# Optimization experiments

Measured on AMD Instinct MI355X. Metric: run time of the kernel, lower is better.

The kernel has to match this reference:

```python
import jax, jax.numpy as jnp
import numpy as np

B, T_ENC, T_DEC = 32, 256, 256
ENC, HID, ATT, CCH, K = 512, 1024, 128, 32, 31
OUT, PRE = 80, 256
ZONEOUT = 0.1
P_DROP = 0.5
PAD = (K - 1) // 2


def setup_inputs() -> dict:
    key = jax.random.key(0)
    ks = jax.random.split(key, 20)
    def n(k, shape, s=0.02):
        return jax.random.normal(k, shape, dtype=jnp.float32) * s
    inp = {}
    inp["encoder_outs"] = jax.random.normal(ks[0], (B, T_ENC, ENC), dtype=jnp.float32)
    inp["decoder_targets"] = jax.random.normal(ks[1], (B, T_DEC, OUT), dtype=jnp.float32)
    keep = 1.0 - P_DROP
    # pre-sampled inverted-dropout masks for the 2 prenet layers at every step
    inp["prenet_masks"] = jax.random.bernoulli(ks[2], keep, (T_DEC, 2, B, PRE)).astype(jnp.float32) / keep
    inp["in_lens"] = jax.random.randint(ks[3], (B,), T_ENC // 2, T_ENC + 1, dtype=jnp.int32)
    # location-sensitive attention params
    inp["V_w"] = n(ks[4], (ATT, ENC)); inp["V_b"] = jnp.zeros((ATT,), jnp.float32)
    inp["W_w"] = n(ks[5], (ATT, HID))
    inp["U_w"] = n(ks[6], (ATT, CCH))
    inp["F_w"] = n(ks[7], (CCH, 1, K))
    inp["w_w"] = n(ks[8], (1, ATT)); inp["w_b"] = jnp.zeros((1,), jnp.float32)
    # prenet
    inp["pre_w0"] = n(ks[9], (PRE, OUT)); inp["pre_b0"] = jnp.zeros((PRE,), jnp.float32)
    inp["pre_w1"] = n(ks[10], (PRE, PRE)); inp["pre_b1"] = jnp.zeros((PRE,), jnp.float32)
    # stacked LSTM cells (zoneout wrappers)
    inp["l0_wih"] = n(ks[11], (4 * HID, ENC + PRE)); inp["l0_whh"] = n(ks[12], (4 * HID, HID))
    inp["l0_bih"] = jnp.zeros((4 * HID,), jnp.float32); inp["l0_bhh"] = jnp.zeros((4 * HID,), jnp.float32)
    inp["l1_wih"] = n(ks[13], (4 * HID, HID)); inp["l1_whh"] = n(ks[14], (4 * HID, HID))
    inp["l1_bih"] = jnp.zeros((4 * HID,), jnp.float32); inp["l1_bhh"] = jnp.zeros((4 * HID,), jnp.float32)
    # output projections
    inp["feat_w"] = n(ks[15], (OUT, ENC + HID))
    inp["prob_w"] = n(ks[16], (1, ENC + HID)); inp["prob_b"] = jnp.zeros((1,), jnp.float32)
    return inp


def _lstm_cell(x, h, c, wih, whh, bih, bhh):
    g = x @ wih.T + bih + h @ whh.T + bhh
    i, f, gg, o = jnp.split(g, 4, axis=1)  # torch LSTMCell gate order
    c2 = jax.nn.sigmoid(f) * c + jax.nn.sigmoid(i) * jnp.tanh(gg)
    h2 = jax.nn.sigmoid(o) * jnp.tanh(c2)
    return h2, c2


def _decode(encoder_outs, decoder_targets, prenet_masks, in_lens,
            V_w, V_b, W_w, U_w, F_w, w_w, w_b,
            pre_w0, pre_b0, pre_w1, pre_b1,
            l0_wih, l0_whh, l0_bih, l0_bhh,
            l1_wih, l1_whh, l1_bih, l1_bhh,
            feat_w, prob_w, prob_b):
    b = encoder_outs.shape[0]
    pad_mask = jnp.arange(T_ENC)[None, :] >= in_lens[:, None]       # [B,T_enc] True = pad
    att_uniform = (~pad_mask).astype(jnp.float32) / in_lens[:, None].astype(jnp.float32)
    processed_memory = encoder_outs @ V_w.T + V_b                   # [B,T_enc,ATT]
    neg = jnp.float32(-1e9)

    # teacher forcing: prev_out at step 0 is the go-frame, then target[t-1]
    targets_prev = jnp.concatenate(
        [jnp.zeros((b, 1, OUT), jnp.float32), decoder_targets[:, :-1]], axis=1)
    xs = (jnp.swapaxes(targets_prev, 0, 1), prenet_masks[:, 0], prenet_masks[:, 1],
          jnp.arange(T_DEC))

    def step(carry, x):
        h0, c0, h1, c1, cum = carry
        prev_out, m0, m1, t = x
        # location-sensitive attention (prev_att_w = None at t=0 -> uniform over valid)
        att_prev = jnp.where(t == 0, att_uniform, cum)              # [B,T_enc]
        f = jax.lax.conv_general_dilated(
            att_prev[:, None, :], F_w, (1,), [(PAD, PAD)],
            dimension_numbers=("NCH", "OIH", "NCH"))                # [B,CCH,T_enc]
        f = jnp.swapaxes(f, 1, 2)                                   # [B,T_enc,CCH]
        erg = jnp.tanh(processed_memory + (h0 @ W_w.T)[:, None, :] + f @ U_w.T)
        erg = (erg @ w_w.T + w_b)[..., 0]                           # [B,T_enc]
        erg = jnp.where(pad_mask, neg, erg)
        aw = jax.nn.softmax(erg, axis=1)
        att_c = jnp.einsum("bt,bte->be", aw, encoder_outs)          # [B,ENC]
        # prenet (dropout always on, via pre-sampled masks)
        p = jax.nn.relu(prev_out @ pre_w0.T + pre_b0) * m0
        p = jax.nn.relu(p @ pre_w1.T + pre_b1) * m1
        xin = jnp.concatenate([att_c, p], axis=1)
        # zoneout LSTM stack (eval-mode zoneout: convex mix of prev/new states)
        h0n, c0n = _lstm_cell(xin, h0, c0, l0_wih, l0_whh, l0_bih, l0_bhh)
        h0 = ZONEOUT * h0 + (1.0 - ZONEOUT) * h0n
        c0 = ZONEOUT * c0 + (1.0 - ZONEOUT) * c0n
        h1n, c1n = _lstm_cell(h0, h1, c1, l1_wih, l1_whh, l1_bih, l1_bhh)
        h1 = ZONEOUT * h1 + (1.0 - ZONEOUT) * h1n
        c1 = ZONEOUT * c1 + (1.0 - ZONEOUT) * c1n
        hcs = jnp.concatenate([h1, att_c], axis=1)                  # [B,HID+ENC]
        out = hcs @ feat_w.T                                        # [B,OUT] (no bias)
        logit = hcs @ prob_w.T + prob_b                             # [B,1]
        return (h0, c0, h1, c1, cum + aw), (out, logit, aw)

    z = jnp.zeros((b, HID), jnp.float32)
    carry0 = (z, z, z, z, jnp.zeros((b, T_ENC), jnp.float32))
    _, (outs, logits, att_ws) = jax.lax.scan(step, carry0, xs)
    outs = jnp.transpose(outs, (1, 2, 0))      # [B,OUT,T_dec]
    logits = logits[..., 0].T                  # [B,T_dec]
    att_ws = jnp.swapaxes(att_ws, 0, 1)        # [B,T_dec,T_enc]
    return outs, logits, att_ws


def reference(encoder_outs, decoder_targets, prenet_masks, in_lens,
              V_w, V_b, W_w, U_w, F_w, w_w, w_b,
              pre_w0, pre_b0, pre_w1, pre_b1,
              l0_wih, l0_whh, l0_bih, l0_bhh,
              l1_wih, l1_whh, l1_bih, l1_bhh,
              feat_w, prob_w, prob_b):
    return _decode(encoder_outs, decoder_targets, prenet_masks, in_lens,
                   V_w, V_b, W_w, U_w, F_w, w_w, w_b,
                   pre_w0, pre_b0, pre_w1, pre_b1,
                   l0_wih, l0_whh, l0_bih, l0_bhh,
                   l1_wih, l1_whh, l1_bih, l1_bhh,
                   feat_w, prob_w, prob_b)
```

## Files before the change

### kernel.cpp

```cpp
#include <hip/hip_runtime.h>

typedef _Float16 half2_t __attribute__((ext_vector_type(2)));
typedef unsigned uint_t;

#define B_    32
#define TE_   256
#define TD_   256
#define ENC_  512
#define HID_  1024
#define ATT_  128
#define OUT_  80
#define PRE_  256

#define LOG_OFF  655360u
#define ATTW_OFF 663552u

#define OFF_PM    0u
#define OFF_P1H   1048576u
#define OFF_M     2097152u
#define OFF_WWH   2101248u
#define OFF_ENCH  2166784u
#define OFF_W0P   4263936u
#define OFF_W1P   7933952u
#define OFF_XC0   12128256u
#define OFF_XC1   12173312u
#define OFF_C0    12206080u
#define OFF_C1    12238848u
#define OFF_CUM   12271616u
#define OFF_ATTC  12279808u
#define OFF_END   12328960u

__device__ __forceinline__ float rcp_f(float x){ return __builtin_amdgcn_rcpf(x); }
__device__ __forceinline__ float sigm(float x){ return rcp_f(1.0f + __expf(-x)); }
__device__ __forceinline__ float tanh_f(float x){ float e = __expf(2.0f*x); return 1.0f - 2.0f*rcp_f(e+1.0f); }

__device__ __forceinline__ uint_t packh2(float a, float b){
  half2_t h; h[0] = (_Float16)a; h[1] = (_Float16)b;
  return __builtin_bit_cast(uint_t, h);
}
__device__ __forceinline__ float dot2f(uint_t w, uint_t x, float c){
#if __has_builtin(__builtin_amdgcn_fdot2)
  return __builtin_amdgcn_fdot2(__builtin_bit_cast(half2_t, w),
                                __builtin_bit_cast(half2_t, x), c, false);
#else
  half2_t a = __builtin_bit_cast(half2_t, w), b = __builtin_bit_cast(half2_t, x);
  return c + (float)a[0]*(float)b[0] + (float)a[1]*(float)b[1];
#endif
}


__global__ void k_init(float* __restrict__ ws){
  unsigned n = OFF_END - OFF_XC0;
  for (unsigned i = blockIdx.x*blockDim.x + threadIdx.x; i < n; i += gridDim.x*blockDim.x)
    ws[OFF_XC0 + i] = 0.f;
}

__global__ void k_precm(const float* __restrict__ Uw, const float* __restrict__ Fw,
                        float* __restrict__ ws){
  float* M = ws + OFF_M;
  for (int idx = threadIdx.x; idx < 128*31; idx += blockDim.x){
    int a = idx / 31, k = idx % 31;
    float s = 0.f;
    for (int c = 0; c < 32; c++) s += Uw[a*32+c]*Fw[c*31+k];
    M[idx] = s;
  }
}

__global__ void k_cvtww(const float* __restrict__ Ww, float* __restrict__ ws){
  uint_t* WWH = (uint_t*)(ws + OFF_WWH);
  int a = blockIdx.x;
  for (int p = threadIdx.x; p < 512; p += blockDim.x)
    WWH[a*512 + p] = packh2(Ww[a*1024 + 2*p], Ww[a*1024 + 2*p + 1]);
}

__global__ void k_packenc(const float* __restrict__ enc, float* __restrict__ ws){
  uint_t* ENCH = (uint_t*)(ws + OFF_ENCH);
  size_t row = blockIdx.x;
  for (int j = threadIdx.x; j < 256; j += blockDim.x)
    ENCH[row*256 + j] = packh2(enc[row*512 + 2*j], enc[row*512 + 2*j + 1]);
}

__global__ void k_packw0(const float* __restrict__ wih, const float* __restrict__ whh,
                         float* __restrict__ ws){
  uint_t* W = (uint_t*)(ws + OFF_W0P);
  size_t r = blockIdx.x;
  for (int p = threadIdx.x; p < 896; p += blockDim.x){
    int k = 2*p;
    const float* src = (k < 768) ? (wih + r*768 + k) : (whh + r*1024 + (k-768));
    W[r*896 + p] = packh2(src[0], src[1]);
  }
}

__global__ void k_packw1(const float* __restrict__ wih, const float* __restrict__ whh,
                         float* __restrict__ ws){
  uint_t* W = (uint_t*)(ws + OFF_W1P);
  size_t r = blockIdx.x;
  for (int p = threadIdx.x; p < 1024; p += blockDim.x){
    int k = 2*p;
    const float* src = (k < 1024) ? (wih + r*1024 + k) : (whh + r*1024 + (k-1024));
    W[r*1024 + p] = packh2(src[0], src[1]);
  }
}

__global__ __launch_bounds__(256) void k_pm(const float* __restrict__ enc,
    const float* __restrict__ Vw, const float* __restrict__ Vb, float* __restrict__ ws){
  float* pm = ws + OFF_PM;
  int b  = blockIdx.x >> 2;
  int s0 = (blockIdx.x & 3) << 6;
  int a  = threadIdx.x & 127;
  int sh = threadIdx.x >> 7;
  __shared__ float Vl[128*65];
  __shared__ float El[64*64];
  float acc[32];
  #pragma unroll
  for (int i=0;i<32;i++) acc[i]=0.f;
  for (int kc=0; kc<ENC_; kc+=64){
    for (int i=threadIdx.x; i<128*64; i+=256){
      int aa = i>>6, kk = i&63;
      Vl[aa*65+kk] = Vw[aa*ENC_ + kc + kk];
    }
    for (int i=threadIdx.x; i<64*64; i+=256){
      int ss = i>>6, kk = i&63;
      El[i] = enc[(size_t)(b*TE_ + s0 + ss)*ENC_ + kc + kk];
    }
    __syncthreads();
    for (int k=0;k<64;k++){
      float va = Vl[a*65+k];
      const float* er = &El[(sh*32)*64 + k];
      #pragma unroll
      for (int s=0;s<32;s++) acc[s] += va * er[s*64];
    }
    __syncthreads();
  }
  float bb = Vb[a];
  for (int s=0;s<32;s++)
    pm[((size_t)b*128 + a)*256 + (s0 + sh*32 + s)] = acc[s] + bb;
}

__global__ __launch_bounds__(256) void k_pre(const float* __restrict__ tgt,
    const float* __restrict__ w0, const float* __restrict__ b0,
    const float* __restrict__ w1, const float* __restrict__ b1,
    const float* __restrict__ masks, float* __restrict__ ws){
  uint_t* P1H = (uint_t*)(ws + OFF_P1H);
  int t = blockIdx.x, j = threadIdx.x;
  __shared__ float xl[32*80];
  __shared__ float p0l[32*256];
  __shared__ float p1s[256*32];
  for (int i=j; i<32*80; i+=256){
    int b = i/80, o = i%80;
    xl[i] = (t==0) ? 0.f : tgt[((size_t)b*TD_ + (t-1))*80 + o];
  }
  __syncthreads();
  {
    float bj = b0[j];
    float w[80];
    #pragma unroll
    for (int o=0;o<80;o++) w[o] = w0[j*80+o];
    for (int b=0;b<32;b++){
      float a0=0,a1=0,a2=0,a3=0;
      const float* x = &xl[b*80];
      #pragma unroll
      for (int o=0;o<80;o+=4){
        a0+=w[o]*x[o]; a1+=w[o+1]*x[o+1]; a2+=w[o+2]*x[o+2]; a3+=w[o+3]*x[o+3];
      }
      float m = masks[(((size_t)t*2+0)*32+b)*256 + j];
      p0l[b*256 + j] = fmaxf(bj+a0+a1+a2+a3, 0.f) * m;
    }
  }
  __syncthreads();
  {
    float bj = b1[j];
    const float4* wr = (const float4*)(w1 + j*256);
    float acc[32];
    #pragma unroll
    for (int i=0;i<32;i++) acc[i]=0.f;
    for (int o4=0;o4<64;o4++){
      float4 w = wr[o4];
      #pragma unroll
      for (int b=0;b<32;b++){
        const float4 xv = *(const float4*)&p0l[b*256 + o4*4];
        acc[b] += w.x*xv.x + w.y*xv.y + w.z*xv.z + w.w*xv.w;
      }
    }
    for (int b=0;b<32;b++){
      float m = masks[(((size_t)t*2+1)*32+b)*256 + j];
      p1s[j*32 + b] = fmaxf(bj+acc[b], 0.f) * m;
    }
  }
  __syncthreads();
  for (int i=j; i<32*128; i+=256){
    int b = i >> 7, jp = i & 127;
    P1H[((size_t)t*32 + b)*128 + jp] = packh2(p1s[(2*jp)*32 + b], p1s[(2*jp+1)*32 + b]);
  }
}


__global__ __launch_bounds__(512) void k_stepa(int t,
    const int* __restrict__ lens, const float* __restrict__ ww, const float* __restrict__ wb,
    const float* __restrict__ featw, const float* __restrict__ probw,
    const float* __restrict__ probb, float* __restrict__ ws, float* __restrict__ out){
  __shared__ __align__(16) uint_t h0l[512];
  __shared__ __align__(16) float Ml[128*32];
  __shared__ __align__(16) float apad[320];
  __shared__ __align__(16) float whl[128];
  __shared__ __align__(16) float wl[128];
  __shared__ __align__(16) float scl[256];
  __shared__ __align__(16) float awl[256];
  __shared__ __align__(16) float redl[128];
  __shared__ __align__(16) float psq[2048];
  __shared__ __align__(16) float redo[512];
  const int blk = blockIdx.x, tid = threadIdx.x;
  const int pc = t & 1, pp = pc ^ 1;
  uint_t* XC0 = (uint_t*)(ws + OFF_XC0);
  uint_t* XC1 = (uint_t*)(ws + OFF_XC1);
  float* ATTC = ws + OFF_ATTC;

  if (blk >= 32){
    if (t < 2) return;
    const int tt = t - 2;
    int ob = blk - 32;
    int b = tid & 31, rr = (tid>>5)&3, ksq = tid>>7;
    int r = ob*4 + rr;
    const float* wr = (r < 80) ? (featw + (size_t)r*1536) : probw;
    const float* acp = ATTC + (size_t)(tt%3)*16384 + b*512;
    float acc = 0.f;
    for (int j=0;j<96;j++){
      int k = ksq*384 + j*4;
      float x0,x1,x2,x3;
      if (k < 1024){
        uint2 hw = *(const uint2*)(XC1 + b*1024 + pc*512 + (k>>1));
        half2_t ha = __builtin_bit_cast(half2_t, hw.x);
        half2_t hb = __builtin_bit_cast(half2_t, hw.y);
        x0 = (float)ha[0]; x1 = (float)ha[1]; x2 = (float)hb[0]; x3 = (float)hb[1];
      } else {
        float4 f = *(const float4*)(acp + (k-1024));
        x0 = f.x; x1 = f.y; x2 = f.z; x3 = f.w;
      }
      if (r <= 80){
        float4 wv = *(const float4*)(wr + k);
        acc += wv.x*x0 + wv.y*x1 + wv.z*x2 + wv.w*x3;
      }
    }
    redo[(rr*4+ksq)*32 + b] = acc;
    __syncthreads();
    if (tid < 128){
      int b2 = tid&31, r2 = tid>>5;
      float vsum = redo[(r2*4+0)*32+b2] + redo[(r2*4+1)*32+b2]
                 + redo[(r2*4+2)*32+b2] + redo[(r2*4+3)*32+b2];
      int rr2 = ob*4 + r2;
      if (rr2 < 80)       out[((size_t)b2*80 + rr2)*256 + tt] = vsum;
      else if (rr2 == 80) out[LOG_OFF + (size_t)b2*256 + tt] = vsum + probb[0];
    }
    return;
  }

  if (t >= TD_) return;
  const int b = blk;
  const int len = lens[b];
  const float* PM = ws + OFF_PM;
  const float* Mg = ws + OFF_M;
  const uint_t* WWH = (const uint_t*)(ws + OFF_WWH);
  const uint_t* ENCH = (const uint_t*)(ws + OFF_ENCH);
  const uint_t* P1H = (const uint_t*)(ws + OFF_P1H);
  float* CUM = ws + OFF_CUM;

  if (tid < 128)
    *(uint4*)(h0l + tid*4) = *(const uint4*)(XC0 + b*1408 + 384 + pp*512 + tid*4);
  for (int i=tid; i<128*31; i+=512) Ml[(i/31)*32 + (i%31)] = Mg[i];
  for (int i=tid; i<288; i+=512){
    int p = i - 15;
    float vv = 0.f;
    if (p >= 0 && p < 256)
      vv = (t==0) ? ((p < len) ? 1.0f/(float)len : 0.f) : CUM[b*256 + p];
    apad[i] = vv;
  }
  if (tid < 128) wl[tid] = ww[tid];
  __syncthreads();
  {
    int ag = tid >> 4, l16 = tid & 15;
    float wv0=0, wv1=0, wv2=0, wv3=0;
    for (int q=0;q<32;q++){
      uint_t xv = h0l[l16 + q*16];
      wv0 = dot2f(WWH[(ag*4+0)*512 + l16 + q*16], xv, wv0);
      wv1 = dot2f(WWH[(ag*4+1)*512 + l16 + q*16], xv, wv1);
      wv2 = dot2f(WWH[(ag*4+2)*512 + l16 + q*16], xv, wv2);
      wv3 = dot2f(WWH[(ag*4+3)*512 + l16 + q*16], xv, wv3);
    }
    float v0, v1;
    { bool up = (l16 & 8) != 0;
      float g0 = up ? wv0 : wv2, k0 = up ? wv2 : wv0;
      float g1 = up ? wv1 : wv3, k1 = up ? wv3 : wv1;
      v0 = k0 + __shfl_xor(g0, 8);
      v1 = k1 + __shfl_xor(g1, 8); }
    { bool up = (l16 & 4) != 0;
      float g = up ? v0 : v1, k = up ? v1 : v0;
      v0 = k + __shfl_xor(g, 4); }
    v0 += __shfl_xor(v0, 2);
    v0 += __shfl_xor(v0, 1);
    if ((l16 & 3) == 0) whl[ag*4 + (l16>>2)] = v0;
  }
  __syncthreads();
  {
    int pg = tid & 63, q = tid >> 6;
    float apw[36];
    #pragma unroll
    for (int i=0;i<36;i+=4) *(float4*)&apw[i] = *(const float4*)&apad[pg*4 + i];
    float part0=0, part1=0, part2=0, part3=0;
    const float* pmb = PM + (size_t)b*128*256;
    for (int aa=0; aa<16; aa++){
      int a = q*16 + aa;
      const float* mr = Ml + a*32;
      float4 pv = *(const float4*)(pmb + (size_t)a*256 + pg*4);
      float wa = whl[a];
      float u0 = pv.x + wa, u1 = pv.y + wa, u2 = pv.z + wa, u3 = pv.w + wa;
      #pragma unroll
      for (int k=0;k<28;k+=4){
        float4 m4 = *(const float4*)(mr + k);
        u0 += m4.x*apw[k]   + m4.y*apw[k+1] + m4.z*apw[k+2] + m4.w*apw[k+3];
        u1 += m4.x*apw[k+1] + m4.y*apw[k+2] + m4.z*apw[k+3] + m4.w*apw[k+4];
        u2 += m4.x*apw[k+2] + m4.y*apw[k+3] + m4.z*apw[k+4] + m4.w*apw[k+5];
        u3 += m4.x*apw[k+3] + m4.y*apw[k+4] + m4.z*apw[k+5] + m4.w*apw[k+6];
      }
      float m28 = mr[28], m29 = mr[29], m30 = mr[30];
      u0 += m28*apw[28] + m29*apw[29] + m30*apw[30];
      u1 += m28*apw[29] + m29*apw[30] + m30*apw[31];
      u2 += m28*apw[30] + m29*apw[31] + m30*apw[32];
      u3 += m28*apw[31] + m29*apw[32] + m30*apw[33];
      float wv = wl[a];
      part0 += tanh_f(u0)*wv; part1 += tanh_f(u1)*wv;
      part2 += tanh_f(u2)*wv; part3 += tanh_f(u3)*wv;
    }
    float4 pp2; pp2.x = part0; pp2.y = part1; pp2.z = part2; pp2.w = part3;
    *(float4*)&psq[tid*4] = pp2;
  }
  __syncthreads();
  if (tid < 256){
    float s = wb[0];
    int pgg = tid >> 2, d = tid & 3;
    #pragma unroll
    for (int qq=0;qq<8;qq++) s += psq[(qq*64 + pgg)*4 + d];
    scl[tid] = (tid >= len) ? -1.0e9f : s;
  }
  __syncthreads();
  if (tid < 128) redl[tid] = fmaxf(scl[tid], scl[tid+128]);
  __syncthreads();
  if (tid < 64){
    float v = fmaxf(redl[tid], redl[tid+64]);
    #pragma unroll
    for (int off=32; off>0; off>>=1) v = fmaxf(v, __shfl_down(v, off));
    if (tid==0) redl[0] = v;
  }
  __syncthreads();
  float mx = redl[0];
  if (tid < 256) awl[tid] = __expf(scl[tid]-mx);
  __syncthreads();
  if (tid < 128) redl[tid] = awl[tid] + awl[tid+128];
  __syncthreads();
  if (tid < 64){
    float v = redl[tid] + redl[tid+64];
    #pragma unroll
    for (int off=32; off>0; off>>=1) v += __shfl_down(v, off);
    if (tid==0) redl[0] = v;
  }
  __syncthreads();
  float inv = rcp_f(redl[0]);
  if (tid < 256){
    float aw = awl[tid]*inv;
    awl[tid] = aw;
    CUM[b*256 + tid] += aw;
    out[ATTW_OFF + ((size_t)b*TD_ + t)*256 + tid] = aw;
  }
  __syncthreads();
  {
    int el = tid & 127, ph = tid >> 7;
    const uint_t* ep = ENCH + ((size_t)b*256 + ph*64)*256 + el*2;
    float c0=0,c1=0,c2=0,c3=0;
    for (int p=0;p<64;p++){
      float a = awl[ph*64 + p];
      uint2 ev = *(const uint2*)(ep + (size_t)p*256);
      half2_t h0v = __builtin_bit_cast(half2_t, ev.x);
      half2_t h1v = __builtin_bit_cast(half2_t, ev.y);
      c0 += a*(float)h0v[0]; c1 += a*(float)h0v[1];
      c2 += a*(float)h1v[0]; c3 += a*(float)h1v[1];
    }
    float4 ca; ca.x=c0; ca.y=c1; ca.z=c2; ca.w=c3;
    *(float4*)&psq[(ph*128 + el)*4] = ca;
  }
  __syncthreads();
  if (tid < 128){
    float4 s = *(const float4*)&psq[tid*4];
    #pragma unroll
    for (int g=1; g<4; g++){
      float4 o = *(const float4*)&psq[(g*128+tid)*4];
      s.x+=o.x; s.y+=o.y; s.z+=o.z; s.w+=o.w;
    }
    *(float4*)(ATTC + (size_t)(t%3)*16384 + b*512 + tid*4) = s;
    XC0[b*1408 + tid*2]     = packh2(s.x, s.y);
    XC0[b*1408 + tid*2 + 1] = packh2(s.z, s.w);
    XC0[b*1408 + 256 + tid] = P1H[((size_t)t*32 + b)*128 + tid];
  }
}


__global__ __launch_bounds__(512, 1) void k_stepb(int t,
    const float* __restrict__ l0bih, const float* __restrict__ l0bhh,
    const float* __restrict__ l1bih, const float* __restrict__ l1bhh,
    float* __restrict__ ws){
  __shared__ __align__(16) uint_t smem[36992];
  float* gs = (float*)(smem + 32896);
  const int tid = threadIdx.x;
  const int pc = t & 1, pp = pc ^ 1;
  const int bp = tid & 15, ul = (tid>>4)&3, kq = tid >> 6;
  const int seg = tid & 15, bq = tid >> 4;
  const int u0 = blockIdx.x*4;
  uint_t* XC0 = (uint_t*)(ws + OFF_XC0);
  uint_t* XC1 = (uint_t*)(ws + OFF_XC1);
  _Float16* XC0h = (_Float16*)XC0;
  _Float16* XC1h = (_Float16*)XC1;
  float* C0 = ws + OFF_C0;
  float* C1 = ws + OFF_C1;
  const uint_t* W0P = (const uint_t*)(ws + OFF_W0P);
  const uint_t* W1P = (const uint_t*)(ws + OFF_W1P);

  if (t < TD_){
    const uint_t* xsrc = XC0 + bq*1408;
    uint_t* xdst = smem + bq*900;
    #pragma unroll
    for (int q=0;q<14;q++){
      int off = (seg + q*16)*4;
      uint4 v;
      if (off < 384) v = *(const uint4*)(xsrc + off);
      else           v = *(const uint4*)(xsrc + 384 + pp*512 + (off-384));
      *(uint4*)(xdst + off) = v;
    }
  }
  __syncthreads();
  if (t < TD_){
    const uint4* xa = (const uint4*)(smem + bp*900 + kq*112);
    const uint4* xb = (const uint4*)(smem + (bp+16)*900 + kq*112);
    const uint4* w4 = (const uint4*)W0P;
    const int rb = (u0 + ul)*224 + kq*28;
    float a00=0,a01=0,a02=0,a03=0, a10=0,a11=0,a12=0,a13=0;
    #pragma unroll 4
    for (int i=0;i<28;i++){
      uint4 xva = xa[i], xvb = xb[i];
      uint4 w0 = w4[rb + 0*229376 + i];
      uint4 w1 = w4[rb + 1*229376 + i];
      uint4 w2 = w4[rb + 2*229376 + i];
      uint4 w3 = w4[rb + 3*229376 + i];
      a00=dot2f(w0.x,xva.x,a00); a00=dot2f(w0.y,xva.y,a00); a00=dot2f(w0.z,xva.z,a00); a00=dot2f(w0.w,xva.w,a00);
      a10=dot2f(w0.x,xvb.x,a10); a10=dot2f(w0.y,xvb.y,a10); a10=dot2f(w0.z,xvb.z,a10); a10=dot2f(w0.w,xvb.w,a10);
      a01=dot2f(w1.x,xva.x,a01); a01=dot2f(w1.y,xva.y,a01); a01=dot2f(w1.z,xva.z,a01); a01=dot2f(w1.w,xva.w,a01);
      a11=dot2f(w1.x,xvb.x,a11); a11=dot2f(w1.y,xvb.y,a11); a11=dot2f(w1.z,xvb.z,a11); a11=dot2f(w1.w,xvb.w,a11);
      a02=dot2f(w2.x,xva.x,a02); a02=dot2f(w2.y,xva.y,a02); a02=dot2f(w2.z,xva.z,a02); a02=dot2f(w2.w,xva.w,a02);
      a12=dot2f(w2.x,xvb.x,a12); a12=dot2f(w2.y,xvb.y,a12); a12=dot2f(w2.z,xvb.z,a12); a12=dot2f(w2.w,xvb.w,a12);
      a03=dot2f(w3.x,xva.x,a03); a03=dot2f(w3.y,xva.y,a03); a03=dot2f(w3.z,xva.z,a03); a03=dot2f(w3.w,xva.w,a03);
      a13=dot2f(w3.x,xvb.x,a13); a13=dot2f(w3.y,xvb.y,a13); a13=dot2f(w3.z,xvb.z,a13); a13=dot2f(w3.w,xvb.w,a13);
    }
    int base = ((kq*4 + ul)*4);
    gs[(base+0)*32 + bp] = a00; gs[(base+0)*32 + bp+16] = a10;
    gs[(base+1)*32 + bp] = a01; gs[(base+1)*32 + bp+16] = a11;
    gs[(base+2)*32 + bp] = a02; gs[(base+2)*32 + bp+16] = a12;
    gs[(base+3)*32 + bp] = a03; gs[(base+3)*32 + bp+16] = a13;
  }
  __syncthreads();
  if (t < TD_ && tid < 128){
    int b = tid & 31, uu = tid >> 5;
    int u = u0 + uu;
    float g4[4];
    #pragma unroll
    for (int g=0; g<4; g++){
      float s = 0.f;
      #pragma unroll
      for (int k2=0;k2<8;k2++) s += gs[((k2*4+uu)*4 + g)*32 + b];
      g4[g] = s + l0bih[g*1024+u] + l0bhh[g*1024+u];
    }
    float c_old = C0[u*32 + b];
    float h_old = (float)XC0h[b*2816 + 768 + pp*1024 + u];
    float cn = sigm(g4[1])*c_old + sigm(g4[0])*tanh_f(g4[2]);
    float hn = sigm(g4[3])*tanh_f(cn);
    C0[u*32 + b] = 0.1f*c_old + 0.9f*cn;
    XC0h[b*2816 + 768 + pc*1024 + u] = (_Float16)(0.1f*h_old + 0.9f*hn);
  }

  if (t >= 1){
    {
      uint_t* xdst = smem + bq*1028;
      #pragma unroll
      for (int q=0;q<16;q++){
        int off = (seg + q*16)*4;
        uint4 v;
        if (off < 512) v = *(const uint4*)(XC0 + bq*1408 + 384 + pp*512 + off);
        else           v = *(const uint4*)(XC1 + bq*1024 + pc*512 + (off-512));
        *(uint4*)(xdst + off) = v;
      }
    }
    __syncthreads();
    {
      const uint4* xa = (const uint4*)(smem + bp*1028 + kq*128);
      const uint4* xb = (const uint4*)(smem + (bp+16)*1028 + kq*128);
      const uint4* w4 = (const uint4*)W1P;
      const int rb = (u0 + ul)*256 + kq*32;
      float a00=0,a01=0,a02=0,a03=0, a10=0,a11=0,a12=0,a13=0;
      #pragma unroll 4
      for (int i=0;i<32;i++){
        uint4 xva = xa[i], xvb = xb[i];
        uint4 w0 = w4[rb + 0*262144 + i];
        uint4 w1 = w4[rb + 1*262144 + i];
        uint4 w2 = w4[rb + 2*262144 + i];
        uint4 w3 = w4[rb + 3*262144 + i];
        a00=dot2f(w0.x,xva.x,a00); a00=dot2f(w0.y,xva.y,a00); a00=dot2f(w0.z,xva.z,a00); a00=dot2f(w0.w,xva.w,a00);
        a10=dot2f(w0.x,xvb.x,a10); a10=dot2f(w0.y,xvb.y,a10); a10=dot2f(w0.z,xvb.z,a10); a10=dot2f(w0.w,xvb.w,a10);
        a01=dot2f(w1.x,xva.x,a01); a01=dot2f(w1.y,xva.y,a01); a01=dot2f(w1.z,xva.z,a01); a01=dot2f(w1.w,xva.w,a01);
        a11=dot2f(w1.x,xvb.x,a11); a11=dot2f(w1.y,xvb.y,a11); a11=dot2f(w1.z,xvb.z,a11); a11=dot2f(w1.w,xvb.w,a11);
        a02=dot2f(w2.x,xva.x,a02); a02=dot2f(w2.y,xva.y,a02); a02=dot2f(w2.z,xva.z,a02); a02=dot2f(w2.w,xva.w,a02);
        a12=dot2f(w2.x,xvb.x,a12); a12=dot2f(w2.y,xvb.y,a12); a12=dot2f(w2.z,xvb.z,a12); a12=dot2f(w2.w,xvb.w,a12);
        a03=dot2f(w3.x,xva.x,a03); a03=dot2f(w3.y,xva.y,a03); a03=dot2f(w3.z,xva.z,a03); a03=dot2f(w3.w,xva.w,a03);
        a13=dot2f(w3.x,xvb.x,a13); a13=dot2f(w3.y,xvb.y,a13); a13=dot2f(w3.z,xvb.z,a13); a13=dot2f(w3.w,xvb.w,a13);
      }
      int base = ((kq*4 + ul)*4);
      gs[(base+0)*32 + bp] = a00; gs[(base+0)*32 + bp+16] = a10;
      gs[(base+1)*32 + bp] = a01; gs[(base+1)*32 + bp+16] = a11;
      gs[(base+2)*32 + bp] = a02; gs[(base+2)*32 + bp+16] = a12;
      gs[(base+3)*32 + bp] = a03; gs[(base+3)*32 + bp+16] = a13;
    }
    __syncthreads();
    if (tid < 128){
      int b = tid & 31, uu = tid >> 5;
      int u = u0 + uu;
      float g4[4];
      #pragma unroll
      for (int g=0; g<4; g++){
        float s = 0.f;
        #pragma unroll
        for (int k2=0;k2<8;k2++) s += gs[((k2*4+uu)*4 + g)*32 + b];
        g4[g] = s + l1bih[g*1024+u] + l1bhh[g*1024+u];
      }
      float c_old = C1[u*32 + b];
      float h_old = (float)XC1h[b*2048 + pc*1024 + u];
      float cn = sigm(g4[1])*c_old + sigm(g4[0])*tanh_f(g4[2]);
      float hn = sigm(g4[3])*tanh_f(cn);
      C1[u*32 + b] = 0.1f*c_old + 0.9f*cn;
      XC1h[b*2048 + pp*1024 + u] = (_Float16)(0.1f*h_old + 0.9f*hn);
    }
  }
}

extern "C" void kernel_launch(void* const* d_in, const int* in_sizes, int n_in,
                              void* d_out, int out_size, void* d_ws, size_t ws_size,
                              hipStream_t stream){
  const float* enc   = (const float*)d_in[0];
  const float* tgt   = (const float*)d_in[1];
  const float* masks = (const float*)d_in[2];
  const int*   lens  = (const int*)  d_in[3];
  const float* Vw    = (const float*)d_in[4];
  const float* Vb    = (const float*)d_in[5];
  const float* Ww    = (const float*)d_in[6];
  const float* Uw    = (const float*)d_in[7];
  const float* Fw    = (const float*)d_in[8];
  const float* ww    = (const float*)d_in[9];
  const float* wb    = (const float*)d_in[10];
  const float* pw0   = (const float*)d_in[11];
  const float* pb0   = (const float*)d_in[12];
  const float* pw1   = (const float*)d_in[13];
  const float* pb1   = (const float*)d_in[14];
  const float* l0wih = (const float*)d_in[15];
  const float* l0whh = (const float*)d_in[16];
  const float* l0bih = (const float*)d_in[17];
  const float* l0bhh = (const float*)d_in[18];
  const float* l1wih = (const float*)d_in[19];
  const float* l1whh = (const float*)d_in[20];
  const float* l1bih = (const float*)d_in[21];
  const float* l1bhh = (const float*)d_in[22];
  const float* featw = (const float*)d_in[23];
  const float* probw = (const float*)d_in[24];
  const float* probb = (const float*)d_in[25];
  float* ws  = (float*)d_ws;
  float* out = (float*)d_out;

  k_init   <<<256, 256,0,stream>>>(ws);
  k_pre    <<<256, 256,0,stream>>>(tgt, pw0, pb0, pw1, pb1, masks, ws);
  k_precm  <<<1,   256,0,stream>>>(Uw, Fw, ws);
  k_cvtww  <<<128, 256,0,stream>>>(Ww, ws);
  k_packenc<<<8192,256,0,stream>>>(enc, ws);
  k_packw0 <<<4096,256,0,stream>>>(l0wih, l0whh, ws);
  k_packw1 <<<4096,256,0,stream>>>(l1wih, l1whh, ws);
  k_pm     <<<128, 256,0,stream>>>(enc, Vw, Vb, ws);

  for (int t = 0; t < TD_; t++){
    k_stepa<<<56, 512,0,stream>>>(t, lens, ww, wb, featw, probw, probb, ws, out);
    k_stepb<<<256,512,0,stream>>>(t, l0bih, l0bhh, l1bih, l1bhh, ws);
  }
  k_stepb<<<256,512,0,stream>>>(256, l0bih, l0bhh, l1bih, l1bhh, ws);
  k_stepa<<<56, 512,0,stream>>>(256, lens, ww, wb, featw, probw, probb, ws, out);
  k_stepa<<<56, 512,0,stream>>>(257, lens, ww, wb, featw, probw, probb, ws, out);
}
```

Measured before the change: 15.56 ms.

## Split LSTM layers across separate blocks and stage weights in LDS; transpose W_w

The step-b kernel now launches twice as many blocks, one half computing layer 0 and the other half layer 1 at the same time, instead of one block doing both layers one after the other. Each block copies its 16 weight rows into LDS and streams the input vector through in 128-element chunks, prefetching the next chunk into registers. The attention W·h product in step-a uses a transposed fp16 weight layout so reads are coalesced across threads, with a small LDS reduction in place of shuffles. Running both layers side by side shortens the serial chain inside each step, at the cost of loading each weight block into LDS on every launch and of more synchronisation.

Result: slower. 15.92 ms (+2.3%).

```diff
diff --git a/kernel.cpp b/kernel.cpp
--- a/kernel.cpp
+++ b/kernel.cpp
@@ -18,7 +18,7 @@
 #define OFF_PM    0u
 #define OFF_P1H   1048576u
 #define OFF_M     2097152u
-#define OFF_WWH   2101248u
+#define OFF_WWHT  2101248u
 #define OFF_ENCH  2166784u
 #define OFF_W0P   4263936u
 #define OFF_W1P   7933952u
@@ -67,10 +67,10 @@
 }
 
 __global__ void k_cvtww(const float* __restrict__ Ww, float* __restrict__ ws){
-  uint_t* WWH = (uint_t*)(ws + OFF_WWH);
-  int a = blockIdx.x;
-  for (int p = threadIdx.x; p < 512; p += blockDim.x)
-    WWH[a*512 + p] = packh2(Ww[a*1024 + 2*p], Ww[a*1024 + 2*p + 1]);
+  uint_t* WT = (uint_t*)(ws + OFF_WWHT);
+  int p = blockIdx.x;
+  for (int a = threadIdx.x; a < 128; a += blockDim.x)
+    WT[p*128 + a] = packh2(Ww[a*1024 + 2*p], Ww[a*1024 + 2*p + 1]);
 }
 
 __global__ void k_packenc(const float* __restrict__ enc, float* __restrict__ ws){
@@ -259,7 +259,7 @@
   const int len = lens[b];
   const float* PM = ws + OFF_PM;
   const float* Mg = ws + OFF_M;
-  const uint_t* WWH = (const uint_t*)(ws + OFF_WWH);
+  const uint_t* WWHT = (const uint_t*)(ws + OFF_WWHT);
   const uint_t* ENCH = (const uint_t*)(ws + OFF_ENCH);
   const uint_t* P1H = (const uint_t*)(ws + OFF_P1H);
   float* CUM = ws + OFF_CUM;
@@ -277,28 +277,19 @@
   if (tid < 128) wl[tid] = ww[tid];
   __syncthreads();
   {
-    int ag = tid >> 4, l16 = tid & 15;
-    float wv0=0, wv1=0, wv2=0, wv3=0;
-    for (int q=0;q<32;q++){
-      uint_t xv = h0l[l16 + q*16];
-      wv0 = dot2f(WWH[(ag*4+0)*512 + l16 + q*16], xv, wv0);
-      wv1 = dot2f(WWH[(ag*4+1)*512 + l16 + q*16], xv, wv1);
-      wv2 = dot2f(WWH[(ag*4+2)*512 + l16 + q*16], xv, wv2);
-      wv3 = dot2f(WWH[(ag*4+3)*512 + l16 + q*16], xv, wv3);
-    }
-    float v0, v1;
-    { bool up = (l16 & 8) != 0;
-      float g0 = up ? wv0 : wv2, k0 = up ? wv2 : wv0;
-      float g1 = up ? wv1 : wv3, k1 = up ? wv3 : wv1;
-      v0 = k0 + __shfl_xor(g0, 8);
-      v1 = k1 + __shfl_xor(g1, 8); }
-    { bool up = (l16 & 4) != 0;
-      float g = up ? v0 : v1, k = up ? v1 : v0;
-      v0 = k + __shfl_xor(g, 4); }
-    v0 += __shfl_xor(v0, 2);
-    v0 += __shfl_xor(v0, 1);
-    if ((l16 & 3) == 0) whl[ag*4 + (l16>>2)] = v0;
-  }
+    int aW = tid & 127, qW = tid >> 7;
+    const uint_t* wt = WWHT + (size_t)(qW*128)*128 + aW;
+    const uint_t* hb = h0l + qW*128;
+    float s0 = 0.f, s1 = 0.f;
+    #pragma unroll 8
+    for (int p=0;p<128;p+=2){
+      s0 = dot2f(wt[(size_t)p*128],     hb[p],   s0);
+      s1 = dot2f(wt[(size_t)(p+1)*128], hb[p+1], s1);
+    }
+    psq[qW*128 + aW] = s0 + s1;
+  }
+  __syncthreads();
+  if (tid < 128) whl[tid] = psq[tid] + psq[128+tid] + psq[256+tid] + psq[384+tid];
   __syncthreads();
   {
     int pg = tid & 63, q = tid >> 6;
@@ -402,127 +393,72 @@
 }
 
 
-__global__ __launch_bounds__(512, 1) void k_stepb(int t,
+__global__ __launch_bounds__(512) void k_stepb(int t,
     const float* __restrict__ l0bih, const float* __restrict__ l0bhh,
     const float* __restrict__ l1bih, const float* __restrict__ l1bhh,
     float* __restrict__ ws){
-  __shared__ __align__(16) uint_t smem[36992];
-  float* gs = (float*)(smem + 32896);
+  __shared__ __align__(16) uint_t lds[16*1028 + 32*132];
+  uint_t* wlds = lds;
+  uint_t* xl   = lds + 16*1028;
+  float*  gs   = (float*)lds;
   const int tid = threadIdx.x;
   const int pc = t & 1, pp = pc ^ 1;
-  const int bp = tid & 15, ul = (tid>>4)&3, kq = tid >> 6;
-  const int seg = tid & 15, bq = tid >> 4;
-  const int u0 = blockIdx.x*4;
+  const int bp = tid & 15, ul = (tid>>4)&3, kq = tid>>6;
+  const int sb = tid >> 4, sp = (tid & 15) * 8;
+  const bool is0 = blockIdx.x < 256;
+  const int u0 = (is0 ? blockIdx.x : blockIdx.x - 256) * 4;
   uint_t* XC0 = (uint_t*)(ws + OFF_XC0);
   uint_t* XC1 = (uint_t*)(ws + OFF_XC1);
   _Float16* XC0h = (_Float16*)XC0;
   _Float16* XC1h = (_Float16*)XC1;
-  float* C0 = ws + OFF_C0;
-  float* C1 = ws + OFF_C1;
-  const uint_t* W0P = (const uint_t*)(ws + OFF_W0P);
-  const uint_t* W1P = (const uint_t*)(ws + OFF_W1P);
-
-  if (t < TD_){
-    const uint_t* xsrc = XC0 + bq*1408;
-    uint_t* xdst = smem + bq*900;
-    #pragma unroll
-    for (int q=0;q<14;q++){
-      int off = (seg + q*16)*4;
-      uint4 v;
-      if (off < 384) v = *(const uint4*)(xsrc + off);
-      else           v = *(const uint4*)(xsrc + 384 + pp*512 + (off-384));
-      *(uint4*)(xdst + off) = v;
-    }
-  }
-  __syncthreads();
-  if (t < TD_){
-    const uint4* xa = (const uint4*)(smem + bp*900 + kq*112);
-    const uint4* xb = (const uint4*)(smem + (bp+16)*900 + kq*112);
-    const uint4* w4 = (const uint4*)W0P;
-    const int rb = (u0 + ul)*224 + kq*28;
-    float a00=0,a01=0,a02=0,a03=0, a10=0,a11=0,a12=0,a13=0;
-    #pragma unroll 4
-    for (int i=0;i<28;i++){
-      uint4 xva = xa[i], xvb = xb[i];
-      uint4 w0 = w4[rb + 0*229376 + i];
-      uint4 w1 = w4[rb + 1*229376 + i];
-      uint4 w2 = w4[rb + 2*229376 + i];
-      uint4 w3 = w4[rb + 3*229376 + i];
-      a00=dot2f(w0.x,xva.x,a00); a00=dot2f(w0.y,xva.y,a00); a00=dot2f(w0.z,xva.z,a00); a00=dot2f(w0.w,xva.w,a00);
-      a10=dot2f(w0.x,xvb.x,a10); a10=dot2f(w0.y,xvb.y,a10); a10=dot2f(w0.z,xvb.z,a10); a10=dot2f(w0.w,xvb.w,a10);
-      a01=dot2f(w1.x,xva.x,a01); a01=dot2f(w1.y,xva.y,a01); a01=dot2f(w1.z,xva.z,a01); a01=dot2f(w1.w,xva.w,a01);
-      a11=dot2f(w1.x,xvb.x,a11); a11=dot2f(w1.y,xvb.y,a11); a11=dot2f(w1.z,xvb.z,a11); a11=dot2f(w1.w,xvb.w,a11);
-      a02=dot2f(w2.x,xva.x,a02); a02=dot2f(w2.y,xva.y,a02); a02=dot2f(w2.z,xva.z,a02); a02=dot2f(w2.w,xva.w,a02);
-      a12=dot2f(w2.x,xvb.x,a12); a12=dot2f(w2.y,xvb.y,a12); a12=dot2f(w2.z,xvb.z,a12); a12=dot2f(w2.w,xvb.w,a12);
-      a03=dot2f(w3.x,xva.x,a03); a03=dot2f(w3.y,xva.y,a03); a03=dot2f(w3.z,xva.z,a03); a03=dot2f(w3.w,xva.w,a03);
-      a13=dot2f(w3.x,xvb.x,a13); a13=dot2f(w3.y,xvb.y,a13); a13=dot2f(w3.z,xvb.z,a13); a13=dot2f(w3.w,xvb.w,a13);
-    }
-    int base = ((kq*4 + ul)*4);
-    gs[(base+0)*32 + bp] = a00; gs[(base+0)*32 + bp+16] = a10;
-    gs[(base+1)*32 + bp] = a01; gs[(base+1)*32 + bp+16] = a11;
-    gs[(base+2)*32 + bp] = a02; gs[(base+2)*32 + bp+16] = a12;
-    gs[(base+3)*32 + bp] = a03; gs[(base+3)*32 + bp+16] = a13;
-  }
-  __syncthreads();
-  if (t < TD_ && tid < 128){
-    int b = tid & 31, uu = tid >> 5;
-    int u = u0 + uu;
-    float g4[4];
+
+  if (is0){
+    if (t >= TD_) return;
+    const uint_t* W0P = (const uint_t*)(ws + OFF_W0P);
+    for (int i=tid; i<16*896; i+=512){
+      int r = i/896, p = i - r*896;
+      wlds[r*904 + p] = W0P[(size_t)((r&3)*1024 + u0 + (r>>2))*896 + p];
+    }
+    float a0[4]={0,0,0,0}, a1[4]={0,0,0,0};
+    uint4 rx0, rx1;
+    { const uint_t* src = XC0 + sb*1408 + sp;
+      rx0 = *(const uint4*)src; rx1 = *(const uint4*)(src+4); }
+    #pragma unroll 1
+    for (int c=0;c<7;c++){
+      __syncthreads();
+      *(uint4*)(xl + sb*132 + sp)     = rx0;
+      *(uint4*)(xl + sb*132 + sp + 4) = rx1;
+      __syncthreads();
+      if (c+1 < 7){
+        int co = (c+1)*128 + sp;
+        const uint_t* src = (co < 384) ? (XC0 + sb*1408 + co)
+                                       : (XC0 + sb*1408 + 384 + pp*512 + (co-384));
+        rx0 = *(const uint4*)src; rx1 = *(const uint4*)(src+4);
+      }
+      const int wb = c*128 + kq*16;
+      const uint_t* xpa = xl + bp*132 + kq*16;
+      const uint_t* xpb = xl + (bp+16)*132 + kq*16;
+      uint2 xa[8], xb[8];
+      #pragma unroll
+      for (int j=0;j<8;j++){ xa[j] = *(const uint2*)(xpa + 2*j); xb[j] = *(const uint2*)(xpb + 2*j); }
+      #pragma unroll
+      for (int g=0; g<4; g++){
+        const uint_t* wr = wlds + (g + 4*ul)*904 + wb;
+        float s0 = a0[g], s1 = a1[g];
+        #pragma unroll
+        for (int j=0;j<8;j++){
+          uint2 w = *(const uint2*)(wr + 2*j);
+          s0 = dot2f(w.x, xa[j].x, s0); s0 = dot2f(w.y, xa[j].y, s0);
+          s1 = dot2f(w.x, xb[j].x, s1); s1 = dot2f(w.y, xb[j].y, s1);
+        }
+        a0[g] = s0; a1[g] = s1;
+      }
+    }
+    __syncthreads();
     #pragma unroll
     for (int g=0; g<4; g++){
-      float s = 0.f;
-      #pragma unroll
-      for (int k2=0;k2<8;k2++) s += gs[((k2*4+uu)*4 + g)*32 + b];
-      g4[g] = s + l0bih[g*1024+u] + l0bhh[g*1024+u];
-    }
-    float c_old = C0[u*32 + b];
-    float h_old = (float)XC0h[b*2816 + 768 + pp*1024 + u];
-    float cn = sigm(g4[1])*c_old + sigm(g4[0])*tanh_f(g4[2]);
-    float hn = sigm(g4[3])*tanh_f(cn);
-    C0[u*32 + b] = 0.1f*c_old + 0.9f*cn;
-    XC0h[b*2816 + 768 + pc*1024 + u] = (_Float16)(0.1f*h_old + 0.9f*hn);
-  }
-
-  if (t >= 1){
-    {
-      uint_t* xdst = smem + bq*1028;
-      #pragma unroll
-      for (int q=0;q<16;q++){
-        int off = (seg + q*16)*4;
-        uint4 v;
-        if (off < 512) v = *(const uint4*)(XC0 + bq*1408 + 384 + pp*512 + off);
-        else           v = *(const uint4*)(XC1 + bq*1024 + pc*512 + (off-512));
-        *(uint4*)(xdst + off) = v;
-      }
-    }
-    __syncthreads();
-    {
-      const uint4* xa = (const uint4*)(smem + bp*1028 + kq*128);
-      const uint4* xb = (const uint4*)(smem + (bp+16)*1028 + kq*128);
-      const uint4* w4 = (const uint4*)W1P;
-      const int rb = (u0 + ul)*256 + kq*32;
-      float a00=0,a01=0,a02=0,a03=0, a10=0,a11=0,a12=0,a13=0;
-      #pragma unroll 4
-      for (int i=0;i<32;i++){
-        uint4 xva = xa[i], xvb = xb[i];
-        uint4 w0 = w4[rb + 0*262144 + i];
-        uint4 w1 = w4[rb + 1*262144 + i];
-        uint4 w2 = w4[rb + 2*262144 + i];
-        uint4 w3 = w4[rb + 3*262144 + i];
-        a00=dot2f(w0.x,xva.x,a00); a00=dot2f(w0.y,xva.y,a00); a00=dot2f(w0.z,xva.z,a00); a00=dot2f(w0.w,xva.w,a00);
-        a10=dot2f(w0.x,xvb.x,a10); a10=dot2f(w0.y,xvb.y,a10); a10=dot2f(w0.z,xvb.z,a10); a10=dot2f(w0.w,xvb.w,a10);
-        a01=dot2f(w1.x,xva.x,a01); a01=dot2f(w1.y,xva.y,a01); a01=dot2f(w1.z,xva.z,a01); a01=dot2f(w1.w,xva.w,a01);
-        a11=dot2f(w1.x,xvb.x,a11); a11=dot2f(w1.y,xvb.y,a11); a11=dot2f(w1.z,xvb.z,a11); a11=dot2f(w1.w,xvb.w,a11);
-        a02=dot2f(w2.x,xva.x,a02); a02=dot2f(w2.y,xva.y,a02); a02=dot2f(w2.z,xva.z,a02); a02=dot2f(w2.w,xva.w,a02);
-        a12=dot2f(w2.x,xvb.x,a12); a12=dot2f(w2.y,xvb.y,a12); a12=dot2f(w2.z,xvb.z,a12); a12=dot2f(w2.w,xvb.w,a12);
-        a03=dot2f(w3.x,xva.x,a03); a03=dot2f(w3.y,xva.y,a03); a03=dot2f(w3.z,xva.z,a03); a03=dot2f(w3.w,xva.w,a03);
-        a13=dot2f(w3.x,xvb.x,a13); a13=dot2f(w3.y,xvb.y,a13); a13=dot2f(w3.z,xvb.z,a13); a13=dot2f(w3.w,xvb.w,a13);
-      }
-      int base = ((kq*4 + ul)*4);
-      gs[(base+0)*32 + bp] = a00; gs[(base+0)*32 + bp+16] = a10;
-      gs[(base+1)*32 + bp] = a01; gs[(base+1)*32 + bp+16] = a11;
-      gs[(base+2)*32 + bp] = a02; gs[(base+2)*32 + bp+16] = a12;
-      gs[(base+3)*32 + bp] = a03; gs[(base+3)*32 + bp+16] = a13;
+      gs[(kq*16 + g + 4*ul)*33 + bp]      = a0[g];
+      gs[(kq*16 + g + 4*ul)*33 + bp + 16] = a1[g];
     }
     __syncthreads();
     if (tid < 128){
@@ -533,14 +469,81 @@
       for (int g=0; g<4; g++){
         float s = 0.f;
         #pragma unroll
-        for (int k2=0;k2<8;k2++) s += gs[((k2*4+uu)*4 + g)*32 + b];
+        for (int k2=0;k2<8;k2++) s += gs[(k2*16 + g + 4*uu)*33 + b];
+        g4[g] = s + l0bih[g*1024+u] + l0bhh[g*1024+u];
+      }
+      float c_old = (ws + OFF_C0)[u*32 + b];
+      float h_old = (float)XC0h[b*2816 + 768 + pp*1024 + u];
+      float cn = sigm(g4[1])*c_old + sigm(g4[0])*tanh_f(g4[2]);
+      float hn = sigm(g4[3])*tanh_f(cn);
+      (ws + OFF_C0)[u*32 + b] = 0.1f*c_old + 0.9f*cn;
+      XC0h[b*2816 + 768 + pc*1024 + u] = (_Float16)(0.1f*h_old + 0.9f*hn);
+    }
+  } else {
+    if (t < 1) return;
+    const uint_t* W1P = (const uint_t*)(ws + OFF_W1P);
+    for (int i=tid; i<16*1024; i+=512){
+      int r = i >> 10, p = i & 1023;
+      wlds[r*1028 + p] = W1P[(size_t)((r&3)*1024 + u0 + (r>>2))*1024 + p];
+    }
+    float a0[4]={0,0,0,0}, a1[4]={0,0,0,0};
+    uint4 rx0, rx1;
+    { const uint_t* src = XC0 + sb*1408 + 384 + pp*512 + sp;
+      rx0 = *(const uint4*)src; rx1 = *(const uint4*)(src+4); }
+    #pragma unroll 1
+    for (int c=0;c<8;c++){
+      __syncthreads();
+      *(uint4*)(xl + sb*132 + sp)     = rx0;
+      *(uint4*)(xl + sb*132 + sp + 4) = rx1;
+      __syncthreads();
+      if (c+1 < 8){
+        int co = (c+1)*128 + sp;
+        const uint_t* src = (co < 512) ? (XC0 + sb*1408 + 384 + pp*512 + co)
+                                       : (XC1 + sb*1024 + pc*512 + (co-512));
+        rx0 = *(const uint4*)src; rx1 = *(const uint4*)(src+4);
+      }
+      const int wb = c*128 + kq*16;
+      const uint_t* xpa = xl + bp*132 + kq*16;
+      const uint_t* xpb = xl + (bp+16)*132 + kq*16;
+      uint2 xa[8], xb[8];
+      #pragma unroll
+      for (int j=0;j<8;j++){ xa[j] = *(const uint2*)(xpa + 2*j); xb[j] = *(const uint2*)(xpb + 2*j); }
+      #pragma unroll
+      for (int g=0; g<4; g++){
+        const uint_t* wr = wlds + (g + 4*ul)*1028 + wb;
+        float s0 = a0[g], s1 = a1[g];
+        #pragma unroll
+        for (int j=0;j<8;j++){
+          uint2 w = *(const uint2*)(wr + 2*j);
+          s0 = dot2f(w.x, xa[j].x, s0); s0 = dot2f(w.y, xa[j].y, s0);
+          s1 = dot2f(w.x, xb[j].x, s1); s1 = dot2f(w.y, xb[j].y, s1);
+        }
+        a0[g] = s0; a1[g] = s1;
+      }
+    }
+    __syncthreads();
+    #pragma unroll
+    for (int g=0; g<4; g++){
+      gs[(kq*16 + g + 4*ul)*33 + bp]      = a0[g];
+      gs[(kq*16 + g + 4*ul)*33 + bp + 16] = a1[g];
+    }
+    __syncthreads();
+    if (tid < 128){
+      int b = tid & 31, uu = tid >> 5;
+      int u = u0 + uu;
+      float g4[4];
+      #pragma unroll
+      for (int g=0; g<4; g++){
+        float s = 0.f;
+        #pragma unroll
+        for (int k2=0;k2<8;k2++) s += gs[(k2*16 + g + 4*uu)*33 + b];
         g4[g] = s + l1bih[g*1024+u] + l1bhh[g*1024+u];
       }
-      float c_old = C1[u*32 + b];
+      float c_old = (ws + OFF_C1)[u*32 + b];
       float h_old = (float)XC1h[b*2048 + pc*1024 + u];
       float cn = sigm(g4[1])*c_old + sigm(g4[0])*tanh_f(g4[2]);
       float hn = sigm(g4[3])*tanh_f(cn);
-      C1[u*32 + b] = 0.1f*c_old + 0.9f*cn;
+      (ws + OFF_C1)[u*32 + b] = 0.1f*c_old + 0.9f*cn;
       XC1h[b*2048 + pp*1024 + u] = (_Float16)(0.1f*h_old + 0.9f*hn);
     }
   }
@@ -581,7 +584,7 @@
   k_init   <<<256, 256,0,stream>>>(ws);
   k_pre    <<<256, 256,0,stream>>>(tgt, pw0, pb0, pw1, pb1, masks, ws);
   k_precm  <<<1,   256,0,stream>>>(Uw, Fw, ws);
-  k_cvtww  <<<128, 256,0,stream>>>(Ww, ws);
+  k_cvtww  <<<512, 128,0,stream>>>(Ww, ws);
   k_packenc<<<8192,256,0,stream>>>(enc, ws);
   k_packw0 <<<4096,256,0,stream>>>(l0wih, l0whh, ws);
   k_packw1 <<<4096,256,0,stream>>>(l1wih, l1whh, ws);
@@ -589,9 +592,9 @@
 
   for (int t = 0; t < TD_; t++){
     k_stepa<<<56, 512,0,stream>>>(t, lens, ww, wb, featw, probw, probb, ws, out);
-    k_stepb<<<256,512,0,stream>>>(t, l0bih, l0bhh, l1bih, l1bhh, ws);
-  }
-  k_stepb<<<256,512,0,stream>>>(256, l0bih, l0bhh, l1bih, l1bhh, ws);
+    k_stepb<<<512,512,0,stream>>>(t, l0bih, l0bhh, l1bih, l1bhh, ws);
+  }
+  k_stepb<<<512,512,0,stream>>>(256, l0bih, l0bhh, l1bih, l1bhh, ws);
   k_stepa<<<56, 512,0,stream>>>(256, lens, ww, wb, featw, probw, probb, ws, out);
   k_stepa<<<56, 512,0,stream>>>(257, lens, ww, wb, featw, probw, probb, ws, out);
 }
```
